# Kernel optimization log

Measured on AMD Instinct MI355X. Metric: run time of the kernel, lower is better.

## Reference

```python
import jax, jax.numpy as jnp
import numpy as np

B, L, S, D, H = 2, 2048, 2048, 256, 8
HD = D // H  # per-head dim = 32
EPS = 1e-5


def _layernorm(x, g, b):
    m = jnp.mean(x, axis=-1, keepdims=True)
    v = jnp.mean(jnp.square(x - m), axis=-1, keepdims=True)
    return (x - m) * jax.lax.rsqrt(v + EPS) * g + b


def setup_inputs() -> dict:
    key = jax.random.key(0)
    ks = jax.random.split(key, 12)
    w = lambda k, o, i: jax.random.normal(k, (o, i), dtype=jnp.float32) * (1.0 / np.sqrt(i))
    return {
        "x": jax.random.normal(ks[0], (B, L, D), dtype=jnp.float32),
        "source": jax.random.normal(ks[1], (B, S, D), dtype=jnp.float32),
        "attn_factor": jax.random.uniform(ks[2], (B, L, S), dtype=jnp.float32),
        "Wq": w(ks[3], D, D),
        "Wk": w(ks[4], D, D),
        "Wv": w(ks[5], D, D),
        "Wm": w(ks[6], D, D),
        "W1": w(ks[7], 2 * D, 2 * D),
        "W2": w(ks[8], D, 2 * D),
        "g1": jnp.ones((D,), jnp.float32),
        "b1": jnp.zeros((D,), jnp.float32),
        "g2": jnp.ones((D,), jnp.float32),
        "b2": jnp.zeros((D,), jnp.float32),
    }


def reference(x, source, attn_factor, Wq, Wk, Wv, Wm, W1, W2, g1, b1, g2, b2):
    bs, l, d = x.shape
    s = source.shape[1]
    # projections (torch Linear: y = x @ W^T), split heads
    qw = (x @ Wq.T).reshape(bs, l, H, HD)       # [B,L,H,hd]
    kw = (source @ Wk.T).reshape(bs, s, H, HD)  # [B,S,H,hd]
    vw = (source @ Wv.T).reshape(bs, s, H, HD)  # [B,S,H,hd]
    # QK^T -> [B,L,S,H], scale, elementwise attn_factor, softmax over S
    a = jnp.einsum("nlhd,nshd->nlsh", qw, kw)
    a = a / np.sqrt(HD)
    a = a * attn_factor[:, :, :, None]
    a = jax.nn.softmax(a, axis=2)
    # AV -> [B,L,H,hd] -> merge heads
    o = jnp.einsum("nlsh,nshd->nlhd", a, vw).reshape(bs, l, d)
    message = o @ Wm.T
    message = _layernorm(message, g1, b1)
    h = jnp.concatenate([x, message], axis=2)       # [B,L,2D]
    h = jnp.maximum(h @ W1.T, 0.0)                  # ReLU MLP
    message = h @ W2.T                              # [B,L,D]
    message = _layernorm(message, g2, b2)
    return x + message
```

## Files before the change

kernel.cpp:

```cpp
#include <hip/hip_runtime.h>
#include <hip/hip_bf16.h>
#include <math.h>

#define B_  2
#define L_  2048
#define S_  2048
#define D_  256
#define H_  8
#define HD_ 32
#define ML_ (B_ * L_)
#define MS_ (B_ * S_)
#define NSPLIT 4
#define SCHUNK (S_ / NSPLIT)

typedef __attribute__((ext_vector_type(8))) short short8;
typedef __attribute__((ext_vector_type(4))) float f32x4;

__global__ __launch_bounds__(256) void convert_all(
    const float* __restrict__ x,  const float* __restrict__ src,
    const float* __restrict__ Wq, const float* __restrict__ Wk,
    const float* __restrict__ Wv, const float* __restrict__ Wm,
    const float* __restrict__ W1, const float* __restrict__ W2,
    __hip_bfloat16* xb,  __hip_bfloat16* srcb,
    __hip_bfloat16* Wqb, __hip_bfloat16* Wkb,
    __hip_bfloat16* Wvb, __hip_bfloat16* Wmb,
    __hip_bfloat16* W1b, __hip_bfloat16* W2b) {
    const size_t i4 = ((size_t)blockIdx.x * 256 + threadIdx.x) * 4;
    const float* sp; __hip_bfloat16* dp; size_t off;
    if      (i4 < 1048576) { sp = x;   dp = xb;   off = i4; }
    else if (i4 < 2097152) { sp = src; dp = srcb; off = i4 - 1048576; }
    else if (i4 < 2162688) { sp = Wq;  dp = Wqb;  off = i4 - 2097152; }
    else if (i4 < 2228224) { sp = Wk;  dp = Wkb;  off = i4 - 2162688; }
    else if (i4 < 2293760) { sp = Wv;  dp = Wvb;  off = i4 - 2228224; }
    else if (i4 < 2359296) { sp = Wm;  dp = Wmb;  off = i4 - 2293760; }
    else if (i4 < 2621440) { sp = W1;  dp = W1b;  off = i4 - 2359296; }
    else                   { sp = W2;  dp = W2b;  off = i4 - 2621440; }
    float4 v = *(const float4*)(sp + off);
    __hip_bfloat16 o0 = __float2bfloat16(v.x), o1 = __float2bfloat16(v.y);
    __hip_bfloat16 o2 = __float2bfloat16(v.z), o3 = __float2bfloat16(v.w);
    __hip_bfloat16* d = dp + off;
    d[0] = o0; d[1] = o1; d[2] = o2; d[3] = o3;
}

template <bool RELU, typename OutT>
__device__ __forceinline__ void gemm_body(const __hip_bfloat16* __restrict__ A,
                                          const __hip_bfloat16* __restrict__ A2,
                                          const __hip_bfloat16* __restrict__ Bm,
                                          OutT* __restrict__ C,
                                          int N, int K, int lda, int m0, int n0,
                                          float cscale,
                                          __hip_bfloat16 (&As)[64][72],
                                          __hip_bfloat16 (&Bs)[64][72]) {
    const int tid  = threadIdx.x;
    const int w    = tid >> 6;
    const int lane = tid & 63;
    const int colL = lane & 15;
    const int quad = lane >> 4;
    const int mh = (w & 1) * 32, nh = (w >> 1) * 32;
    const int srow = tid >> 3;
    const int scg  = (tid & 7) * 8;

    f32x4 acc[2][2] = {};

    auto loadA = [&](int p, int k0) -> short8 {
        const __hip_bfloat16* Asrc = A; int kk = k0;
        if (A2 && k0 >= 256) { Asrc = A2; kk = k0 - 256; }
        return *(const short8*)(Asrc + (size_t)(m0 + srow + p * 32) * lda + kk + scg);
    };
    auto loadB = [&](int p, int k0) -> short8 {
        return *(const short8*)(Bm + (size_t)(n0 + srow + p * 32) * K + k0 + scg);
    };

    short8 ra[2], rb[2];
#pragma unroll
    for (int p = 0; p < 2; ++p) { ra[p] = loadA(p, 0); rb[p] = loadB(p, 0); }

    for (int k0 = 0; k0 < K; k0 += 64) {
        __syncthreads();
#pragma unroll
        for (int p = 0; p < 2; ++p) {
            *(short8*)&As[srow + p * 32][scg] = ra[p];
            *(short8*)&Bs[srow + p * 32][scg] = rb[p];
        }
        __syncthreads();
        if (k0 + 64 < K) {
#pragma unroll
            for (int p = 0; p < 2; ++p) { ra[p] = loadA(p, k0 + 64); rb[p] = loadB(p, k0 + 64); }
        }
#pragma unroll
        for (int ks = 0; ks < 2; ++ks) {
            short8 af[2], bf[2];
#pragma unroll
            for (int i = 0; i < 2; ++i)
                af[i] = *(const short8*)&As[mh + i * 16 + colL][ks * 32 + quad * 8];
#pragma unroll
            for (int j = 0; j < 2; ++j)
                bf[j] = *(const short8*)&Bs[nh + j * 16 + colL][ks * 32 + quad * 8];
#pragma unroll
            for (int i = 0; i < 2; ++i)
#pragma unroll
                for (int j = 0; j < 2; ++j)
                    acc[i][j] = __builtin_amdgcn_mfma_f32_16x16x32_bf16(af[i], bf[j], acc[i][j], 0, 0, 0);
        }
    }
#pragma unroll
    for (int i = 0; i < 2; ++i)
#pragma unroll
        for (int r = 0; r < 4; ++r) {
            const size_t row = m0 + mh + i * 16 + quad * 4 + r;
#pragma unroll
            for (int j = 0; j < 2; ++j) {
                float v = acc[i][j][r] * cscale;
                if (RELU) v = fmaxf(v, 0.f);
                C[row * N + n0 + nh + j * 16 + colL] = (OutT)v;
            }
        }
}

__global__ __launch_bounds__(256) void proj_fused(const __hip_bfloat16* __restrict__ x_b,
                                                  const __hip_bfloat16* __restrict__ src_b,
                                                  const __hip_bfloat16* __restrict__ Wq_b,
                                                  const __hip_bfloat16* __restrict__ Wk_b,
                                                  const __hip_bfloat16* __restrict__ Wv_b,
                                                  __hip_bfloat16* __restrict__ Qb,
                                                  __hip_bfloat16* __restrict__ Kb,
                                                  __hip_bfloat16* __restrict__ Vtb) {
    __shared__ __hip_bfloat16 As[64][72];
    __shared__ __hip_bfloat16 Bs[64][72];
    const int id = blockIdx.x;
    if (id < 256) {
        gemm_body<false, __hip_bfloat16>(x_b, nullptr, Wq_b, Qb, 256, 256, 256,
                                         (id >> 2) * 64, (id & 3) * 64,
                                         0.17677669529663687f, As, Bs);
    } else if (id < 512) {
        const int t = id - 256;
        gemm_body<false, __hip_bfloat16>(src_b, nullptr, Wk_b, Kb, 256, 256, 256,
                                         (t >> 2) * 64, (t & 3) * 64, 1.f, As, Bs);
    } else {
        const int t = id - 512;
        const int b = t >> 7, u = t & 127;
        gemm_body<false, __hip_bfloat16>(Wv_b, nullptr, src_b + (size_t)b * S_ * D_,
                                         Vtb + (size_t)b * D_ * S_, S_, 256, 256,
                                         (u & 3) * 64, (u >> 2) * 64, 1.f, As, Bs);
    }
}

__global__ __launch_bounds__(256, 4) void attn_mfma(const __hip_bfloat16* __restrict__ Qb,
                                                    const __hip_bfloat16* __restrict__ Kb,
                                                    const __hip_bfloat16* __restrict__ Vtb,
                                                    const float* __restrict__ F,
                                                    __hip_bfloat16* __restrict__ Op,
                                                    float* __restrict__ Ll) {
    const int tid  = threadIdx.x;
    const int w    = tid >> 6;
    const int lane = tid & 63;
    const int colL = lane & 15;
    const int quad = lane >> 4;

    const int b     = blockIdx.z >> 2;
    const int split = blockIdx.z & 3;
    const int h     = blockIdx.y;
    const int qw    = blockIdx.x * 64 + w * 16;

    __shared__ __hip_bfloat16 Ks[128][40];
    __shared__ __hip_bfloat16 Vs[32][136];
    __shared__ __hip_bfloat16 Pw[4][16][72];

    const short8 aq = *(const short8*)(Qb + ((size_t)(b * L_ + qw + colL)) * D_ + h * HD_ + quad * 8);

    float lsum[4] = {0.f, 0.f, 0.f, 0.f};
    f32x4 o0 = {0.f, 0.f, 0.f, 0.f}, o1 = {0.f, 0.f, 0.f, 0.f};

    const int kr = tid >> 2, kc = (tid & 3) * 8;
    const int vr = tid >> 3, vc = (tid & 7) * 8;
    const __hip_bfloat16* kst = Kb + ((size_t)(b * S_ + kr)) * D_ + h * HD_ + kc;
    const __hip_bfloat16* vst = Vtb + (size_t)b * D_ * S_ + ((size_t)(h * HD_ + vr)) * S_ + vc;
    const float* fbase = F + ((size_t)(b * L_ + qw + quad * 4)) * S_ + colL;

    const int sbeg = split * SCHUNK, send = sbeg + SCHUNK;
    short8 rk[2], rv[2];
#pragma unroll
    for (int p = 0; p < 2; ++p) {
        rk[p] = *(const short8*)(kst + (size_t)(sbeg + p * 64) * D_);
        rv[p] = *(const short8*)(vst + sbeg + p * 64);
    }

    for (int s0 = sbeg; s0 < send; s0 += 128) {
        __syncthreads();
        *(short8*)&Ks[kr][kc]        = rk[0];
        *(short8*)&Ks[kr + 64][kc]   = rk[1];
        *(short8*)&Vs[vr][vc]        = rv[0];
        *(short8*)&Vs[vr][vc + 64]   = rv[1];
        __syncthreads();
        if (s0 + 128 < send) {
#pragma unroll
            for (int p = 0; p < 2; ++p) {
                rk[p] = *(const short8*)(kst + (size_t)(s0 + 128 + p * 64) * D_);
                rv[p] = *(const short8*)(vst + s0 + 128 + p * 64);
            }
        }
#pragma unroll
        for (int hs = 0; hs < 2; ++hs) {
            const int sh = s0 + hs * 64;
            f32x4 cc[4];
#pragma unroll
            for (int n = 0; n < 4; ++n) {
                short8 kf = *(const short8*)&Ks[hs * 64 + n * 16 + colL][quad * 8];
                f32x4 z = {0.f, 0.f, 0.f, 0.f};
                cc[n] = __builtin_amdgcn_mfma_f32_16x16x32_bf16(aq, kf, z, 0, 0, 0);
            }
#pragma unroll
            for (int n = 0; n < 4; ++n)
#pragma unroll
                for (int r = 0; r < 4; ++r) {
                    float fv = fbase[(size_t)r * S_ + sh + n * 16];
                    float p = __expf(cc[n][r] * fv);
                    lsum[r] += p;
                    Pw[w][quad * 4 + r][n * 16 + colL] = __float2bfloat16(p);
                }
            short8 a0 = *(const short8*)(&Pw[w][colL][quad * 8]);
            short8 a1 = *(const short8*)(&Pw[w][colL][32 + quad * 8]);
#pragma unroll
            for (int ks = 0; ks < 2; ++ks) {
                short8 ap = ks ? a1 : a0;
#pragma unroll
                for (int nt = 0; nt < 2; ++nt) {
                    short8 vf = *(const short8*)&Vs[nt * 16 + colL][hs * 64 + ks * 32 + quad * 8];
                    if (nt == 0) o0 = __builtin_amdgcn_mfma_f32_16x16x32_bf16(ap, vf, o0, 0, 0, 0);
                    else         o1 = __builtin_amdgcn_mfma_f32_16x16x32_bf16(ap, vf, o1, 0, 0, 0);
                }
            }
        }
    }

#pragma unroll
    for (int r = 0; r < 4; ++r) {
        float t = lsum[r];
        t += __shfl_xor(t, 1);
        t += __shfl_xor(t, 2);
        t += __shfl_xor(t, 4);
        t += __shfl_xor(t, 8);
        lsum[r] = t;
    }

#pragma unroll
    for (int r = 0; r < 4; ++r) {
        const size_t row = (size_t)(b * L_ + qw + quad * 4 + r);
        const size_t po = ((size_t)split * ML_ + row) * D_ + h * HD_;
        Op[po + colL]      = __float2bfloat16(o0[r]);
        Op[po + 16 + colL] = __float2bfloat16(o1[r]);
        if (colL == 0)
            Ll[((size_t)split * H_ + h) * ML_ + row] = lsum[r];
    }
}

__global__ __launch_bounds__(512) void mlp_fused(const __hip_bfloat16* __restrict__ Opart,
                                                 const float* __restrict__ Ll,
                                                 const __hip_bfloat16* __restrict__ x_b,
                                                 const __hip_bfloat16* __restrict__ Wm_b,
                                                 const __hip_bfloat16* __restrict__ W1_b,
                                                 const __hip_bfloat16* __restrict__ W2_b,
                                                 const float* __restrict__ g1,
                                                 const float* __restrict__ b1,
                                                 const float* __restrict__ g2,
                                                 const float* __restrict__ b2,
                                                 const float* __restrict__ x,
                                                 float* __restrict__ out) {
    __shared__ __hip_bfloat16 Bs[256][72];
    __shared__ __hip_bfloat16 As[16][72];
    __shared__ __hip_bfloat16 Acat[16][520];
    __shared__ __hip_bfloat16 Hs[16][520];
    __shared__ float gs[256], bs_[256];
    __shared__ float stats[8][16][2];
    __shared__ float Linv[16][8];

    const int tid  = threadIdx.x;
    const int w    = tid >> 6;
    const int lane = tid & 63;
    const int colL = lane & 15;
    const int quad = lane >> 4;
    const int nh   = w * 32;
    const int m0   = blockIdx.x * 16;
    const int srow = tid >> 3;
    const int scg  = (tid & 7) * 8;

    if (tid < 256) { gs[tid] = g1[tid]; bs_[tid] = b1[tid]; }
    if (tid < 128) {
        const int row = tid >> 3, hh = tid & 7;
        float t = 0.f;
#pragma unroll
        for (int s = 0; s < NSPLIT; ++s)
            t += Ll[((size_t)s * H_ + hh) * ML_ + m0 + row];
        Linv[row][hh] = 1.f / t;
    }
    if (tid < 256) {
        const int xr = tid >> 4, xc = (tid & 15) * 16;
        *(short8*)&Acat[xr][xc]     = *(const short8*)(x_b + (size_t)(m0 + xr) * 256 + xc);
        *(short8*)&Acat[xr][xc + 8] = *(const short8*)(x_b + (size_t)(m0 + xr) * 256 + xc + 8);
    }
    __syncthreads();

    f32x4 acc[2] = {};
    auto loadA1 = [&](int k0) -> short8 {
        const float inv = Linv[srow][(k0 + scg) >> 5];
        float a[8] = {};
#pragma unroll
        for (int s = 0; s < NSPLIT; ++s) {
            short8 v = *(const short8*)(Opart + ((size_t)s * ML_ + m0 + srow) * 256 + k0 + scg);
#pragma unroll
            for (int e = 0; e < 8; ++e) {
                union { short s16; __hip_bfloat16 h; } c; c.s16 = v[e];
                a[e] += __bfloat162float(c.h);
            }
        }
        short8 outv;
#pragma unroll
        for (int e = 0; e < 8; ++e) {
            union { __hip_bfloat16 h; short s16; } c;
            c.h = __float2bfloat16(a[e] * inv);
            outv[e] = c.s16;
        }
        return outv;
    };

    {
        short8 ra = {};
        if (srow < 16) ra = loadA1(0);
        short8 rb[4];
#pragma unroll
        for (int p = 0; p < 4; ++p)
            rb[p] = *(const short8*)(Wm_b + (size_t)(srow + p * 64) * 256 + scg);
        for (int k0 = 0; k0 < 256; k0 += 64) {
            __syncthreads();
            if (srow < 16) *(short8*)&As[srow][scg] = ra;
#pragma unroll
            for (int p = 0; p < 4; ++p)
                *(short8*)&Bs[srow + p * 64][scg] = rb[p];
            __syncthreads();
            if (k0 + 64 < 256) {
                if (srow < 16) ra = loadA1(k0 + 64);
#pragma unroll
                for (int p = 0; p < 4; ++p)
                    rb[p] = *(const short8*)(Wm_b + (size_t)(srow + p * 64) * 256 + k0 + 64 + scg);
            }
#pragma unroll
            for (int ks = 0; ks < 2; ++ks) {
                short8 af = *(const short8*)&As[colL][ks * 32 + quad * 8];
#pragma unroll
                for (int j = 0; j < 2; ++j) {
                    short8 bf = *(const short8*)&Bs[nh + j * 16 + colL][ks * 32 + quad * 8];
                    acc[j] = __builtin_amdgcn_mfma_f32_16x16x32_bf16(af, bf, acc[j], 0, 0, 0);
                }
            }
        }
    }
#pragma unroll
    for (int r = 0; r < 4; ++r) {
        float s = 0.f, q = 0.f;
#pragma unroll
        for (int j = 0; j < 2; ++j) { float v = acc[j][r]; s += v; q += v * v; }
        s += __shfl_xor(s, 1); q += __shfl_xor(q, 1);
        s += __shfl_xor(s, 2); q += __shfl_xor(q, 2);
        s += __shfl_xor(s, 4); q += __shfl_xor(q, 4);
        s += __shfl_xor(s, 8); q += __shfl_xor(q, 8);
        if (colL == 0) { stats[w][quad * 4 + r][0] = s; stats[w][quad * 4 + r][1] = q; }
    }
    __syncthreads();
#pragma unroll
    for (int r = 0; r < 4; ++r) {
        const int row = quad * 4 + r;
        float S = 0.f, Q = 0.f;
#pragma unroll
        for (int ww = 0; ww < 8; ++ww) { S += stats[ww][row][0]; Q += stats[ww][row][1]; }
        const float mean = S * (1.f / 256.f);
        const float rstd = rsqrtf(Q * (1.f / 256.f) - mean * mean + 1e-5f);
#pragma unroll
        for (int j = 0; j < 2; ++j) {
            const int col = nh + j * 16 + colL;
            Acat[row][256 + col] = __float2bfloat16((acc[j][r] - mean) * rstd * gs[col] + bs_[col]);
        }
    }
    __syncthreads();

#pragma unroll 1
    for (int nc = 0; nc < 2; ++nc) {
#pragma unroll
        for (int j = 0; j < 2; ++j) acc[j] = (f32x4){0.f, 0.f, 0.f, 0.f};
        short8 rb[4];
#pragma unroll
        for (int p = 0; p < 4; ++p)
            rb[p] = *(const short8*)(W1_b + (size_t)(nc * 256 + srow + p * 64) * 512 + scg);
        for (int k0 = 0; k0 < 512; k0 += 64) {
            __syncthreads();
#pragma unroll
            for (int p = 0; p < 4; ++p)
                *(short8*)&Bs[srow + p * 64][scg] = rb[p];
            __syncthreads();
            if (k0 + 64 < 512) {
#pragma unroll
                for (int p = 0; p < 4; ++p)
                    rb[p] = *(const short8*)(W1_b + (size_t)(nc * 256 + srow + p * 64) * 512 + k0 + 64 + scg);
            }
#pragma unroll
            for (int ks = 0; ks < 2; ++ks) {
                short8 af = *(const short8*)&Acat[colL][k0 + ks * 32 + quad * 8];
#pragma unroll
                for (int j = 0; j < 2; ++j) {
                    short8 bf = *(const short8*)&Bs[nh + j * 16 + colL][ks * 32 + quad * 8];
                    acc[j] = __builtin_amdgcn_mfma_f32_16x16x32_bf16(af, bf, acc[j], 0, 0, 0);
                }
            }
        }
#pragma unroll
        for (int r = 0; r < 4; ++r) {
            const int row = quad * 4 + r;
#pragma unroll
            for (int j = 0; j < 2; ++j) {
                const int col = nc * 256 + nh + j * 16 + colL;
                Hs[row][col] = __float2bfloat16(fmaxf(acc[j][r], 0.f));
            }
        }
    }
    if (tid < 256) { gs[tid] = g2[tid]; bs_[tid] = b2[tid]; }
    __syncthreads();

#pragma unroll
    for (int j = 0; j < 2; ++j) acc[j] = (f32x4){0.f, 0.f, 0.f, 0.f};
    {
        short8 rb[4];
#pragma unroll
        for (int p = 0; p < 4; ++p)
            rb[p] = *(const short8*)(W2_b + (size_t)(srow + p * 64) * 512 + scg);
        for (int k0 = 0; k0 < 512; k0 += 64) {
            __syncthreads();
#pragma unroll
            for (int p = 0; p < 4; ++p)
                *(short8*)&Bs[srow + p * 64][scg] = rb[p];
            __syncthreads();
            if (k0 + 64 < 512) {
#pragma unroll
                for (int p = 0; p < 4; ++p)
                    rb[p] = *(const short8*)(W2_b + (size_t)(srow + p * 64) * 512 + k0 + 64 + scg);
            }
#pragma unroll
            for (int ks = 0; ks < 2; ++ks) {
                short8 af = *(const short8*)&Hs[colL][k0 + ks * 32 + quad * 8];
#pragma unroll
                for (int j = 0; j < 2; ++j) {
                    short8 bf = *(const short8*)&Bs[nh + j * 16 + colL][ks * 32 + quad * 8];
                    acc[j] = __builtin_amdgcn_mfma_f32_16x16x32_bf16(af, bf, acc[j], 0, 0, 0);
                }
            }
        }
    }
#pragma unroll
    for (int r = 0; r < 4; ++r) {
        float s = 0.f, q = 0.f;
#pragma unroll
        for (int j = 0; j < 2; ++j) { float v = acc[j][r]; s += v; q += v * v; }
        s += __shfl_xor(s, 1); q += __shfl_xor(q, 1);
        s += __shfl_xor(s, 2); q += __shfl_xor(q, 2);
        s += __shfl_xor(s, 4); q += __shfl_xor(q, 4);
        s += __shfl_xor(s, 8); q += __shfl_xor(q, 8);
        if (colL == 0) { stats[w][quad * 4 + r][0] = s; stats[w][quad * 4 + r][1] = q; }
    }
    __syncthreads();
#pragma unroll
    for (int r = 0; r < 4; ++r) {
        const int row = quad * 4 + r;
        float S = 0.f, Q = 0.f;
#pragma unroll
        for (int ww = 0; ww < 8; ++ww) { S += stats[ww][row][0]; Q += stats[ww][row][1]; }
        const float mean = S * (1.f / 256.f);
        const float rstd = rsqrtf(Q * (1.f / 256.f) - mean * mean + 1e-5f);
        const size_t grow = (size_t)(m0 + row) * 256;
#pragma unroll
        for (int j = 0; j < 2; ++j) {
            const int col = nh + j * 16 + colL;
            out[grow + col] = (acc[j][r] - mean) * rstd * gs[col] + bs_[col] + x[grow + col];
        }
    }
}

extern "C" void kernel_launch(void* const* d_in, const int* in_sizes, int n_in,
                              void* d_out, int out_size, void* d_ws, size_t ws_size,
                              hipStream_t stream) {
    (void)in_sizes; (void)n_in; (void)out_size; (void)ws_size;
    const float* x   = (const float*)d_in[0];
    const float* src = (const float*)d_in[1];
    const float* F   = (const float*)d_in[2];
    const float* Wq  = (const float*)d_in[3];
    const float* Wk  = (const float*)d_in[4];
    const float* Wv  = (const float*)d_in[5];
    const float* Wm  = (const float*)d_in[6];
    const float* W1  = (const float*)d_in[7];
    const float* W2  = (const float*)d_in[8];
    const float* g1  = (const float*)d_in[9];
    const float* b1  = (const float*)d_in[10];
    const float* g2  = (const float*)d_in[11];
    const float* b2  = (const float*)d_in[12];
    float* out = (float*)d_out;

    char* ws = (char*)d_ws;
    __hip_bfloat16* x_b   = (__hip_bfloat16*)(ws);
    __hip_bfloat16* src_b = (__hip_bfloat16*)(ws + (2u << 20));
    __hip_bfloat16* Wq_b  = (__hip_bfloat16*)(ws + (4u << 20));
    __hip_bfloat16* Wk_b  = (__hip_bfloat16*)(ws + (4u << 20) + 131072);
    __hip_bfloat16* Wv_b  = (__hip_bfloat16*)(ws + (4u << 20) + 2 * 131072);
    __hip_bfloat16* Wm_b  = (__hip_bfloat16*)(ws + (4u << 20) + 3 * 131072);
    __hip_bfloat16* W1_b  = (__hip_bfloat16*)(ws + (4u << 20) + 4 * 131072);
    __hip_bfloat16* W2_b  = (__hip_bfloat16*)(ws + (4u << 20) + 4 * 131072 + 524288);
    __hip_bfloat16* Qb   = (__hip_bfloat16*)(ws + (6u << 20));
    __hip_bfloat16* Kb   = (__hip_bfloat16*)(ws + (8u << 20));
    __hip_bfloat16* Vtb  = (__hip_bfloat16*)(ws + (10u << 20));
    __hip_bfloat16* Opart = (__hip_bfloat16*)(ws + (14u << 20));
    float* Ll  = (float*)(ws + (22u << 20));

    dim3 blk(256);
    convert_all<<<dim3(2688), blk, 0, stream>>>(x, src, Wq, Wk, Wv, Wm, W1, W2,
                                                x_b, src_b, Wq_b, Wk_b, Wv_b, Wm_b, W1_b, W2_b);
    proj_fused<<<dim3(768), blk, 0, stream>>>(x_b, src_b, Wq_b, Wk_b, Wv_b, Qb, Kb, Vtb);
    attn_mfma<<<dim3(L_ / 64, H_, B_ * NSPLIT), blk, 0, stream>>>(Qb, Kb, Vtb, F, Opart, Ll);
    mlp_fused<<<dim3(ML_ / 16), dim3(512), 0, stream>>>(Opart, Ll, x_b, Wm_b, W1_b, W2_b,
                                                        g1, b1, g2, b2, x, out);
}
```

Measured before the change: 159.0 us.

## Load MLP weight fragments directly from global instead of staging through LDS

The fused MLP kernel no longer stages the Wm, W1 and W2 tiles through shared memory with double-buffered register prefetch and per-tile barriers. Each wave now reads its B fragments straight from global (L2-cached) memory and runs the K loop fully unrolled. The attention output reduction and normalization are also precomputed once into a shared A tile. The goal is to remove many __syncthreads and LDS round-trips and cut shared-memory use so occupancy can rise, at the cost of uncoalesced 16-byte global loads with no explicit prefetch. An unused A2 argument is also dropped from the projection GEMM.

```diff
diff --git a/kernel.cpp b/kernel.cpp
--- a/kernel.cpp
+++ b/kernel.cpp
@@ -44,7 +44,6 @@
 
 template <bool RELU, typename OutT>
 __device__ __forceinline__ void gemm_body(const __hip_bfloat16* __restrict__ A,
-                                          const __hip_bfloat16* __restrict__ A2,
                                           const __hip_bfloat16* __restrict__ Bm,
                                           OutT* __restrict__ C,
                                           int N, int K, int lda, int m0, int n0,
@@ -63,9 +62,7 @@
     f32x4 acc[2][2] = {};
 
     auto loadA = [&](int p, int k0) -> short8 {
-        const __hip_bfloat16* Asrc = A; int kk = k0;
-        if (A2 && k0 >= 256) { Asrc = A2; kk = k0 - 256; }
-        return *(const short8*)(Asrc + (size_t)(m0 + srow + p * 32) * lda + kk + scg);
+        return *(const short8*)(A + (size_t)(m0 + srow + p * 32) * lda + k0 + scg);
     };
     auto loadB = [&](int p, int k0) -> short8 {
         return *(const short8*)(Bm + (size_t)(n0 + srow + p * 32) * K + k0 + scg);
@@ -129,17 +126,17 @@
     __shared__ __hip_bfloat16 Bs[64][72];
     const int id = blockIdx.x;
     if (id < 256) {
-        gemm_body<false, __hip_bfloat16>(x_b, nullptr, Wq_b, Qb, 256, 256, 256,
+        gemm_body<false, __hip_bfloat16>(x_b, Wq_b, Qb, 256, 256, 256,
                                          (id >> 2) * 64, (id & 3) * 64,
                                          0.17677669529663687f, As, Bs);
     } else if (id < 512) {
         const int t = id - 256;
-        gemm_body<false, __hip_bfloat16>(src_b, nullptr, Wk_b, Kb, 256, 256, 256,
+        gemm_body<false, __hip_bfloat16>(src_b, Wk_b, Kb, 256, 256, 256,
                                          (t >> 2) * 64, (t & 3) * 64, 1.f, As, Bs);
     } else {
         const int t = id - 512;
         const int b = t >> 7, u = t & 127;
-        gemm_body<false, __hip_bfloat16>(Wv_b, nullptr, src_b + (size_t)b * S_ * D_,
+        gemm_body<false, __hip_bfloat16>(Wv_b, src_b + (size_t)b * S_ * D_,
                                          Vtb + (size_t)b * D_ * S_, S_, 256, 256,
                                          (u & 3) * 64, (u >> 2) * 64, 1.f, As, Bs);
     }
@@ -266,13 +263,11 @@
                                                  const float* __restrict__ b2,
                                                  const float* __restrict__ x,
                                                  float* __restrict__ out) {
-    __shared__ __hip_bfloat16 Bs[256][72];
-    __shared__ __hip_bfloat16 As[16][72];
+    __shared__ __hip_bfloat16 Ac[16][264];
     __shared__ __hip_bfloat16 Acat[16][520];
     __shared__ __hip_bfloat16 Hs[16][520];
     __shared__ float gs[256], bs_[256];
     __shared__ float stats[8][16][2];
-    __shared__ float Linv[16][8];
 
     const int tid  = threadIdx.x;
     const int w    = tid >> 6;
@@ -281,77 +276,51 @@
     const int quad = lane >> 4;
     const int nh   = w * 32;
     const int m0   = blockIdx.x * 16;
-    const int srow = tid >> 3;
-    const int scg  = (tid & 7) * 8;
 
     if (tid < 256) { gs[tid] = g1[tid]; bs_[tid] = b1[tid]; }
-    if (tid < 128) {
-        const int row = tid >> 3, hh = tid & 7;
+    {
+        const int xr = tid >> 5;
+        const int xc = (tid & 31) * 8;
+        *(short8*)&Acat[xr][xc] = *(const short8*)(x_b + (size_t)(m0 + xr) * 256 + xc);
+    }
+    {
+        const int row = tid >> 5;
+        const int cg  = (tid & 31) * 8;
+        const int hh  = cg >> 5;
         float t = 0.f;
 #pragma unroll
         for (int s = 0; s < NSPLIT; ++s)
             t += Ll[((size_t)s * H_ + hh) * ML_ + m0 + row];
-        Linv[row][hh] = 1.f / t;
-    }
-    if (tid < 256) {
-        const int xr = tid >> 4, xc = (tid & 15) * 16;
-        *(short8*)&Acat[xr][xc]     = *(const short8*)(x_b + (size_t)(m0 + xr) * 256 + xc);
-        *(short8*)&Acat[xr][xc + 8] = *(const short8*)(x_b + (size_t)(m0 + xr) * 256 + xc + 8);
-    }
-    __syncthreads();
-
-    f32x4 acc[2] = {};
-    auto loadA1 = [&](int k0) -> short8 {
-        const float inv = Linv[srow][(k0 + scg) >> 5];
+        const float inv = 1.f / t;
         float a[8] = {};
 #pragma unroll
         for (int s = 0; s < NSPLIT; ++s) {
-            short8 v = *(const short8*)(Opart + ((size_t)s * ML_ + m0 + srow) * 256 + k0 + scg);
+            short8 v = *(const short8*)(Opart + ((size_t)s * ML_ + m0 + row) * 256 + cg);
 #pragma unroll
             for (int e = 0; e < 8; ++e) {
                 union { short s16; __hip_bfloat16 h; } c; c.s16 = v[e];
                 a[e] += __bfloat162float(c.h);
             }
         }
-        short8 outv;
+        short8 ov;
 #pragma unroll
         for (int e = 0; e < 8; ++e) {
             union { __hip_bfloat16 h; short s16; } c;
             c.h = __float2bfloat16(a[e] * inv);
-            outv[e] = c.s16;
-        }
-        return outv;
-    };
-
-    {
-        short8 ra = {};
-        if (srow < 16) ra = loadA1(0);
-        short8 rb[4];
-#pragma unroll
-        for (int p = 0; p < 4; ++p)
-            rb[p] = *(const short8*)(Wm_b + (size_t)(srow + p * 64) * 256 + scg);
-        for (int k0 = 0; k0 < 256; k0 += 64) {
-            __syncthreads();
-            if (srow < 16) *(short8*)&As[srow][scg] = ra;
-#pragma unroll
-            for (int p = 0; p < 4; ++p)
-                *(short8*)&Bs[srow + p * 64][scg] = rb[p];
-            __syncthreads();
-            if (k0 + 64 < 256) {
-                if (srow < 16) ra = loadA1(k0 + 64);
-#pragma unroll
-                for (int p = 0; p < 4; ++p)
-                    rb[p] = *(const short8*)(Wm_b + (size_t)(srow + p * 64) * 256 + k0 + 64 + scg);
-            }
-#pragma unroll
-            for (int ks = 0; ks < 2; ++ks) {
-                short8 af = *(const short8*)&As[colL][ks * 32 + quad * 8];
-#pragma unroll
-                for (int j = 0; j < 2; ++j) {
-                    short8 bf = *(const short8*)&Bs[nh + j * 16 + colL][ks * 32 + quad * 8];
-                    acc[j] = __builtin_amdgcn_mfma_f32_16x16x32_bf16(af, bf, acc[j], 0, 0, 0);
-                }
-            }
+            ov[e] = c.s16;
+        }
+        *(short8*)&Ac[row][cg] = ov;
+    }
+    __syncthreads();
+
+    f32x4 acc[2] = {};
+#pragma unroll
+    for (int ks = 0; ks < 8; ++ks) {
+        short8 af = *(const short8*)&Ac[colL][ks * 32 + quad * 8];
+#pragma unroll
+        for (int j = 0; j < 2; ++j) {
+            short8 bf = *(const short8*)(Wm_b + (size_t)(nh + j * 16 + colL) * 256 + ks * 32 + quad * 8);
+            acc[j] = __builtin_amdgcn_mfma_f32_16x16x32_bf16(af, bf, acc[j], 0, 0, 0);
         }
     }
 #pragma unroll
@@ -384,31 +353,14 @@
 
 #pragma unroll 1
     for (int nc = 0; nc < 2; ++nc) {
-#pragma unroll
-        for (int j = 0; j < 2; ++j) acc[j] = (f32x4){0.f, 0.f, 0.f, 0.f};
-        short8 rb[4];
-#pragma unroll
-        for (int p = 0; p < 4; ++p)
-            rb[p] = *(const short8*)(W1_b + (size_t)(nc * 256 + srow + p * 64) * 512 + scg);
-        for (int k0 = 0; k0 < 512; k0 += 64) {
-            __syncthreads();
-#pragma unroll
-            for (int p = 0; p < 4; ++p)
-                *(short8*)&Bs[srow + p * 64][scg] = rb[p];
-            __syncthreads();
-            if (k0 + 64 < 512) {
-#pragma unroll
-                for (int p = 0; p < 4; ++p)
-                    rb[p] = *(const short8*)(W1_b + (size_t)(nc * 256 + srow + p * 64) * 512 + k0 + 64 + scg);
-            }
-#pragma unroll
-            for (int ks = 0; ks < 2; ++ks) {
-                short8 af = *(const short8*)&Acat[colL][k0 + ks * 32 + quad * 8];
-#pragma unroll
-                for (int j = 0; j < 2; ++j) {
-                    short8 bf = *(const short8*)&Bs[nh + j * 16 + colL][ks * 32 + quad * 8];
-                    acc[j] = __builtin_amdgcn_mfma_f32_16x16x32_bf16(af, bf, acc[j], 0, 0, 0);
-                }
+        f32x4 a2[2] = {};
+#pragma unroll
+        for (int ks = 0; ks < 16; ++ks) {
+            short8 af = *(const short8*)&Acat[colL][ks * 32 + quad * 8];
+#pragma unroll
+            for (int j = 0; j < 2; ++j) {
+                short8 bf = *(const short8*)(W1_b + (size_t)(nc * 256 + nh + j * 16 + colL) * 512 + ks * 32 + quad * 8);
+                a2[j] = __builtin_amdgcn_mfma_f32_16x16x32_bf16(af, bf, a2[j], 0, 0, 0);
             }
         }
 #pragma unroll
@@ -417,7 +369,7 @@
 #pragma unroll
             for (int j = 0; j < 2; ++j) {
                 const int col = nc * 256 + nh + j * 16 + colL;
-                Hs[row][col] = __float2bfloat16(fmaxf(acc[j][r], 0.f));
+                Hs[row][col] = __float2bfloat16(fmaxf(a2[j][r], 0.f));
             }
         }
     }
@@ -426,31 +378,13 @@
 
 #pragma unroll
     for (int j = 0; j < 2; ++j) acc[j] = (f32x4){0.f, 0.f, 0.f, 0.f};
-    {
-        short8 rb[4];
-#pragma unroll
-        for (int p = 0; p < 4; ++p)
-            rb[p] = *(const short8*)(W2_b + (size_t)(srow + p * 64) * 512 + scg);
-        for (int k0 = 0; k0 < 512; k0 += 64) {
-            __syncthreads();
-#pragma unroll
-            for (int p = 0; p < 4; ++p)
-                *(short8*)&Bs[srow + p * 64][scg] = rb[p];
-            __syncthreads();
-            if (k0 + 64 < 512) {
-#pragma unroll
-                for (int p = 0; p < 4; ++p)
-                    rb[p] = *(const short8*)(W2_b + (size_t)(srow + p * 64) * 512 + k0 + 64 + scg);
-            }
-#pragma unroll
-            for (int ks = 0; ks < 2; ++ks) {
-                short8 af = *(const short8*)&Hs[colL][k0 + ks * 32 + quad * 8];
-#pragma unroll
-                for (int j = 0; j < 2; ++j) {
-                    short8 bf = *(const short8*)&Bs[nh + j * 16 + colL][ks * 32 + quad * 8];
-                    acc[j] = __builtin_amdgcn_mfma_f32_16x16x32_bf16(af, bf, acc[j], 0, 0, 0);
-                }
-            }
+#pragma unroll
+    for (int ks = 0; ks < 16; ++ks) {
+        short8 af = *(const short8*)&Hs[colL][ks * 32 + quad * 8];
+#pragma unroll
+        for (int j = 0; j < 2; ++j) {
+            short8 bf = *(const short8*)(W2_b + (size_t)(nh + j * 16 + colL) * 512 + ks * 32 + quad * 8);
+            acc[j] = __builtin_amdgcn_mfma_f32_16x16x32_bf16(af, bf, acc[j], 0, 0, 0);
         }
     }
 #pragma unroll
```

Result: slower. 165.2 us (+3.9%).
